# Kernel tuning notes

Measured on AMD Instinct MI355X. Metric: run time of the kernel, lower is better.

Reference implementation:

```python
import jax, jax.numpy as jnp
import numpy as np


def _rbf(X1, X2, log_ls):
    # exp(-||x1-x2||^2 / (2*ls^2)) via the squared-norm expansion
    sq1 = jnp.sum(X1 * X1, axis=-1)[:, None]
    sq2 = jnp.sum(X2 * X2, axis=-1)[None, :]
    d2 = jnp.maximum(sq1 + sq2 - 2.0 * (X1 @ X2.T), 0.0)
    ls2 = jnp.exp(2.0 * log_ls)
    return jnp.exp(-d2 / (2.0 * ls2))


def setup_inputs() -> dict:
    key = jax.random.key(0)
    k1, k2, k3 = jax.random.split(key, 3)
    N_way, K_shot, Q_query, D = 16, 32, 4096, 1024
    Zs = jax.random.normal(k1, (N_way * K_shot, D), dtype=jnp.float32)
    Ys = jax.random.randint(k2, (N_way * K_shot, 1), 0, N_way)
    Zq = jax.random.normal(k3, (N_way * Q_query, D), dtype=jnp.float32)
    log_ls = jnp.asarray(0.0, dtype=jnp.float32)
    log_noise = jnp.asarray(-3.0, dtype=jnp.float32)
    return {"Zs": Zs, "Ys": Ys, "Zq": Zq, "log_ls": log_ls,
            "log_noise": log_noise, "N_way": N_way}


def reference(Zs, Ys, Zq, log_ls, log_noise, N_way):
    Nsamp = Zs.shape[0]  # N_way * K_shot
    Y1hot = jax.nn.one_hot(Ys.reshape(-1), N_way, dtype=Zs.dtype)  # [Nsamp, N_way]
    noise = jnp.exp(2.0 * log_noise)
    Kss = _rbf(Zs, Zs, log_ls) + noise * jnp.eye(Nsamp, dtype=Zs.dtype)
    L = jnp.linalg.cholesky(Kss)
    alpha = jax.scipy.linalg.cho_solve((L, True), Y1hot)  # [Nsamp, N_way]
    Kqs = _rbf(Zq, Zs, log_ls)  # [Q, Nsamp]
    f_q = Kqs @ alpha  # [Q, N_way]
    return jax.nn.softmax(f_q, axis=-1)
```

## Files before the change

### kernel.cpp

```cpp
#include <hip/hip_runtime.h>
#include <math.h>

#define NS 512
#define NQ 65536
#define DD 1024
#define NW 16

typedef __attribute__((ext_vector_type(8))) short short8x;
typedef __attribute__((ext_vector_type(4))) float floatx4;

static __device__ __forceinline__ unsigned short bf_trunc(float x) {
  return (unsigned short)(__float_as_uint(x) >> 16);
}
static __device__ __forceinline__ float bf_tof(unsigned short h) {
  return __uint_as_float(((unsigned)h) << 16);
}
static __device__ __forceinline__ unsigned short bf_rne(float x) {
  unsigned u = __float_as_uint(x);
  return (unsigned short)((u + 0x7FFFu + ((u >> 16) & 1u)) >> 16);
}

#define STASH(Hp, Lp, row, k0, v) do {                                      \
    unsigned e_ = (unsigned)((((row) * 32 + (k0)) ^ (((row) & 7) << 3)));   \
    ushort4 h_, l_;                                                         \
    h_.x = bf_trunc((v).x); l_.x = bf_trunc((v).x - bf_tof(h_.x));          \
    h_.y = bf_trunc((v).y); l_.y = bf_trunc((v).y - bf_tof(h_.y));          \
    h_.z = bf_trunc((v).z); l_.z = bf_trunc((v).z - bf_tof(h_.z));          \
    h_.w = bf_trunc((v).w); l_.w = bf_trunc((v).w - bf_tof(h_.w));          \
    *(ushort4*)&Hp[e_] = h_; *(ushort4*)&Lp[e_] = l_;                       \
  } while (0)

__global__ void row_norms_kernel(const float* __restrict__ X, float* __restrict__ out, int nrows) {
  int gw = (int)((blockIdx.x * blockDim.x + threadIdx.x) >> 6);
  int lane = threadIdx.x & 63;
  if (gw >= nrows) return;
  const float* row = X + (size_t)gw * DD;
  float s = 0.f;
  #pragma unroll
  for (int i = 0; i < 4; ++i) {
    float4 v = *(const float4*)(row + 4 * lane + 256 * i);
    s += v.x * v.x + v.y * v.y + v.z * v.z + v.w * v.w;
  }
  #pragma unroll
  for (int off = 32; off; off >>= 1) s += __shfl_xor(s, off);
  if (lane == 0) out[gw] = s;
}

__global__ __launch_bounds__(256) void kss_kernel(const float* __restrict__ Zs,
                                                  const float* __restrict__ sn,
                                                  const float* __restrict__ log_ls,
                                                  const float* __restrict__ log_noise,
                                                  float* __restrict__ K) {
  __shared__ __align__(16) float At[16][68];
  __shared__ __align__(16) float Bt[16][68];
  int tid = threadIdx.x;
  int rb = blockIdx.y * 64, cb = blockIdx.x * 64;
  int tx = tid & 15, ty = tid >> 4;
  int srow = tid & 63, skq = (tid >> 6) << 2;
  float acc[4][4] = {};
  for (int kk = 0; kk < DD; kk += 16) {
    __syncthreads();
    float4 a = *(const float4*)(Zs + (size_t)(rb + srow) * DD + kk + skq);
    float4 b = *(const float4*)(Zs + (size_t)(cb + srow) * DD + kk + skq);
    At[skq + 0][srow] = a.x; At[skq + 1][srow] = a.y; At[skq + 2][srow] = a.z; At[skq + 3][srow] = a.w;
    Bt[skq + 0][srow] = b.x; Bt[skq + 1][srow] = b.y; Bt[skq + 2][srow] = b.z; Bt[skq + 3][srow] = b.w;
    __syncthreads();
    #pragma unroll
    for (int k = 0; k < 16; ++k) {
      float4 av = *(const float4*)&At[k][ty * 4];
      float4 bv = *(const float4*)&Bt[k][tx * 4];
      float aa[4] = {av.x, av.y, av.z, av.w};
      float bb[4] = {bv.x, bv.y, bv.z, bv.w};
      #pragma unroll
      for (int i = 0; i < 4; ++i)
        #pragma unroll
        for (int j = 0; j < 4; ++j)
          acc[i][j] = fmaf(aa[i], bb[j], acc[i][j]);
    }
  }
  float inv2 = 0.5f * expf(-2.f * log_ls[0]);
  float noise = expf(2.f * log_noise[0]);
  #pragma unroll
  for (int i = 0; i < 4; ++i)
    #pragma unroll
    for (int j = 0; j < 4; ++j) {
      int r = rb + ty * 4 + i, c = cb + tx * 4 + j;
      float d2 = fmaxf(sn[r] + sn[c] - 2.f * acc[i][j], 0.f);
      float v = expf(-d2 * inv2);
      if (r == c) v += noise;
      K[(size_t)r * NS + c] = v;
    }
}

__global__ __launch_bounds__(256) void panel_v2(float* __restrict__ K, int j) {
  __shared__ float Ld[64][68];
  __shared__ float idia_s[64];
  const int tid = threadIdx.x;

  if (tid < 64) {
    const int r = tid;
    float ar[64];
    #pragma unroll
    for (int c4 = 0; c4 < 16; ++c4)
      *(floatx4*)&ar[c4 * 4] = *(const floatx4*)(K + (size_t)(j + r) * NS + j + c4 * 4);
    float myinv = 0.f;
    #pragma unroll
    for (int c = 0; c < 64; ++c) {
      float colv = ar[c];
      float d = __shfl(colv, c);
      float sq = sqrtf(d);
      float inv = 1.f / sq;
      float x = (r > c) ? colv * inv : ((r == c) ? sq : 0.f);
      ar[c] = x;
      if (r == c) myinv = inv;
      #pragma unroll
      for (int k = c + 1; k < 64; ++k) {
        float xk = __shfl(x, k);
        ar[k] = fmaf(-x, xk, ar[k]);
      }
    }
    idia_s[r] = myinv;
    #pragma unroll
    for (int c4 = 0; c4 < 16; ++c4)
      *(floatx4*)&Ld[r][c4 * 4] = *(const floatx4*)&ar[c4 * 4];
    #pragma unroll
    for (int c = 0; c < 64; ++c) {
      if (c <= r) K[(size_t)(j + r) * NS + j + c] = ar[c];
      if (c < r)  K[(size_t)(j + c) * NS + j + r] = ar[c];
    }
  }
  __syncthreads();

  for (int r0 = j + 64 + tid; r0 < NS; r0 += 256) {
    float xr[64];
    #pragma unroll
    for (int c4 = 0; c4 < 16; ++c4)
      *(floatx4*)&xr[c4 * 4] = *(const floatx4*)(K + (size_t)r0 * NS + j + c4 * 4);
    #pragma unroll
    for (int g = 0; g < 16; ++g) {
      float v0 = xr[4 * g + 0], v1 = xr[4 * g + 1], v2 = xr[4 * g + 2], v3 = xr[4 * g + 3];
      for (int kb = 0; kb < g; ++kb) {
        floatx4 x4 = *(const floatx4*)&xr[4 * kb];
        floatx4 l0 = *(const floatx4*)&Ld[4 * g + 0][4 * kb];
        floatx4 l1 = *(const floatx4*)&Ld[4 * g + 1][4 * kb];
        floatx4 l2 = *(const floatx4*)&Ld[4 * g + 2][4 * kb];
        floatx4 l3 = *(const floatx4*)&Ld[4 * g + 3][4 * kb];
        v0 -= x4.x * l0.x + x4.y * l0.y + x4.z * l0.z + x4.w * l0.w;
        v1 -= x4.x * l1.x + x4.y * l1.y + x4.z * l1.z + x4.w * l1.w;
        v2 -= x4.x * l2.x + x4.y * l2.y + x4.z * l2.z + x4.w * l2.w;
        v3 -= x4.x * l3.x + x4.y * l3.y + x4.z * l3.z + x4.w * l3.w;
      }
      const int c0 = 4 * g;
      float x0 = v0 * idia_s[c0 + 0];
      v1 -= x0 * Ld[c0 + 1][c0];
      float x1 = v1 * idia_s[c0 + 1];
      v2 -= x0 * Ld[c0 + 2][c0] + x1 * Ld[c0 + 2][c0 + 1];
      float x2 = v2 * idia_s[c0 + 2];
      v3 -= x0 * Ld[c0 + 3][c0] + x1 * Ld[c0 + 3][c0 + 1] + x2 * Ld[c0 + 3][c0 + 2];
      float x3 = v3 * idia_s[c0 + 3];
      xr[c0 + 0] = x0; xr[c0 + 1] = x1; xr[c0 + 2] = x2; xr[c0 + 3] = x3;
    }
    #pragma unroll
    for (int c4 = 0; c4 < 16; ++c4)
      *(floatx4*)(K + (size_t)r0 * NS + j + c4 * 4) = *(const floatx4*)&xr[c4 * 4];
    #pragma unroll
    for (int c = 0; c < 64; ++c)
      K[(size_t)(j + c) * NS + r0] = xr[c];
  }
}

__global__ __launch_bounds__(256) void syrk_trailing(float* __restrict__ K, int j) {
  int t0 = j + 64;
  int rbt = t0 + blockIdx.y * 64, cbt = t0 + blockIdx.x * 64;
  if (cbt > rbt) return;
  __shared__ float A[64][69];
  __shared__ float B[64][69];
  int tid = threadIdx.x;
  for (int i = tid; i < 64 * 64; i += 256) {
    int r = i >> 6, k = i & 63;
    A[r][k] = K[(size_t)(rbt + r) * NS + j + k];
    B[r][k] = K[(size_t)(cbt + r) * NS + j + k];
  }
  __syncthreads();
  int tx = tid & 15, ty = tid >> 4;
  float acc[4][4] = {};
  for (int k = 0; k < 64; ++k) {
    float aa[4], bb[4];
    #pragma unroll
    for (int i = 0; i < 4; ++i) aa[i] = A[ty * 4 + i][k];
    #pragma unroll
    for (int i = 0; i < 4; ++i) bb[i] = B[tx * 4 + i][k];
    #pragma unroll
    for (int i = 0; i < 4; ++i)
      #pragma unroll
      for (int jj = 0; jj < 4; ++jj)
        acc[i][jj] = fmaf(aa[i], bb[jj], acc[i][jj]);
  }
  #pragma unroll
  for (int i = 0; i < 4; ++i)
    #pragma unroll
    for (int jj = 0; jj < 4; ++jj)
      K[(size_t)(rbt + ty * 4 + i) * NS + cbt + tx * 4 + jj] -= acc[i][jj];
}

__global__ __launch_bounds__(1024) void cho_solve_v2(const float* __restrict__ K,
                                                     const int* __restrict__ Ys,
                                                     unsigned short* __restrict__ alpha_t) {
  __shared__ float P[64][68];
  __shared__ float WsT[16][68];
  __shared__ float Wblk[64][16];
  __shared__ float invd[64];
  const int tid = threadIdx.x;
  const int rs = tid >> 4, nn = tid & 15;
  const int pc = nn * 4;

  float w[8];
  #pragma unroll
  for (int k = 0; k < 8; ++k) w[k] = (Ys[rs + 64 * k] == nn) ? 1.f : 0.f;

  for (int jb = 0; jb < 8; ++jb) {
    const int j = jb << 6;
    __syncthreads();
    #pragma unroll
    for (int k = 0; k < 8; ++k) if (k == jb) Wblk[rs][nn] = w[k];
    *(floatx4*)&P[rs][pc] = *(const floatx4*)(K + (size_t)(j + rs) * NS + j + pc);
    __syncthreads();
    if (tid < 64) {
      const int n = tid & 15, rq = tid >> 4;
      invd[tid] = 1.f / P[tid][tid];
      float w16[16];
      #pragma unroll
      for (int i = 0; i < 16; ++i) w16[i] = Wblk[rq + 4 * i][n];
      #pragma unroll
      for (int g = 0; g < 16; ++g) {
        floatx4 p[16];
        #pragma unroll
        for (int i = 0; i < 16; ++i) p[i] = *(const floatx4*)&P[rq + 4 * i][4 * g];
        #pragma unroll
        for (int cj = 0; cj < 4; ++cj) {
          const int c = 4 * g + cj;
          float xc = __shfl(w16[c >> 2], ((c & 3) << 4) + n) * invd[c];
          if (rq == (c & 3)) w16[c >> 2] = xc;
          #pragma unroll
          for (int i = 0; i < 16; ++i) {
            int r = rq + 4 * i;
            if (r > c) w16[i] -= p[i][cj] * xc;
          }
        }
      }
      #pragma unroll
      for (int i = 0; i < 16; ++i) WsT[n][rq + 4 * i] = w16[i];
    }
    __syncthreads();
    #pragma unroll
    for (int k = 0; k < 8; ++k) if (k == jb) w[k] = WsT[nn][rs];
    floatx4 wsr[16];
    #pragma unroll
    for (int g = 0; g < 16; ++g) wsr[g] = *(const floatx4*)&WsT[nn][4 * g];
    #pragma unroll
    for (int k = 0; k < 8; ++k) {
      if (k > jb) {
        const float* lrow = K + (size_t)(rs + 64 * k) * NS + j;
        float s = w[k];
        #pragma unroll
        for (int g = 0; g < 16; ++g) {
          floatx4 lv = *(const floatx4*)(lrow + 4 * g);
          s -= lv.x * wsr[g].x + lv.y * wsr[g].y + lv.z * wsr[g].z + lv.w * wsr[g].w;
        }
        w[k] = s;
      }
    }
  }

  for (int jb = 7; jb >= 0; --jb) {
    const int j = jb << 6;
    __syncthreads();
    #pragma unroll
    for (int k = 0; k < 8; ++k) if (k == jb) Wblk[rs][nn] = w[k];
    *(floatx4*)&P[rs][pc] = *(const floatx4*)(K + (size_t)(j + rs) * NS + j + pc);
    __syncthreads();
    if (tid < 64) {
      const int n = tid & 15, rq = tid >> 4;
      invd[tid] = 1.f / P[tid][tid];
      float w16[16];
      #pragma unroll
      for (int i = 0; i < 16; ++i) w16[i] = Wblk[rq + 4 * i][n];
      #pragma unroll
      for (int g = 15; g >= 0; --g) {
        floatx4 p[16];
        #pragma unroll
        for (int i = 0; i < 16; ++i) p[i] = *(const floatx4*)&P[rq + 4 * i][4 * g];
        #pragma unroll
        for (int cj = 3; cj >= 0; --cj) {
          const int c = 4 * g + cj;
          float xc = __shfl(w16[c >> 2], ((c & 3) << 4) + n) * invd[c];
          if (rq == (c & 3)) w16[c >> 2] = xc;
          #pragma unroll
          for (int i = 0; i < 16; ++i) {
            int r = rq + 4 * i;
            if (r < c) w16[i] -= p[i][cj] * xc;
          }
        }
      }
      #pragma unroll
      for (int i = 0; i < 16; ++i) WsT[n][rq + 4 * i] = w16[i];
    }
    __syncthreads();
    #pragma unroll
    for (int k = 0; k < 8; ++k) if (k == jb) w[k] = WsT[nn][rs];
    floatx4 wsr[16];
    #pragma unroll
    for (int g = 0; g < 16; ++g) wsr[g] = *(const floatx4*)&WsT[nn][4 * g];
    #pragma unroll
    for (int k = 0; k < 8; ++k) {
      if (k < jb) {
        const float* lrow = K + (size_t)(rs + 64 * k) * NS + j;
        float s = w[k];
        #pragma unroll
        for (int g = 0; g < 16; ++g) {
          floatx4 lv = *(const floatx4*)(lrow + 4 * g);
          s -= lv.x * wsr[g].x + lv.y * wsr[g].y + lv.z * wsr[g].z + lv.w * wsr[g].w;
        }
        w[k] = s;
      }
    }
  }

  #pragma unroll
  for (int k = 0; k < 8; ++k)
    alpha_t[(size_t)nn * NS + rs + 64 * k] = bf_rne(w[k]);
}

__global__ __launch_bounds__(512) void fused_v2(const float* __restrict__ Zq,
                                                const float* __restrict__ Zs,
                                                const float* __restrict__ sn,
                                                const unsigned short* __restrict__ alpha_t,
                                                const float* __restrict__ log_ls,
                                                float* __restrict__ out) {
  __shared__ __align__(16) unsigned short LB[32768];
  __shared__ float qnl[128];
  __shared__ float snl[256];
  unsigned short* AhB = LB;
  unsigned short* AlB = LB + 4096;
  unsigned short* BhB = LB + 8192;
  unsigned short* BlB = LB + 16384;
  unsigned short* KqB = LB;

  const int tid = threadIdx.x;
  const int lane = tid & 63;
  const int w = tid >> 6;
  const int wm = w >> 2, wn = w & 3;
  const int l15 = lane & 15, l4 = lane >> 4;
  const int rb = blockIdx.x * 128;
  const float inv2 = 0.5f * __expf(-2.f * log_ls[0]);
  const unsigned swz = (unsigned)((l15 & 7) << 3);

  if (tid < 128) qnl[tid] = 0.f;
  __syncthreads();

  const int qrow0 = tid >> 3;
  const int qk0 = (tid & 7) * 4;
  const int qrow1 = 64 + qrow0;

  floatx4 facc = {0.f, 0.f, 0.f, 0.f};

  for (int cc = 0; cc < NS; cc += 256) {
    if (tid < 256) snl[tid] = sn[cc + tid];
    floatx4 acc[4][4];
    #pragma unroll
    for (int a = 0; a < 4; ++a)
      #pragma unroll
      for (int b = 0; b < 4; ++b) acc[a][b] = (floatx4){0.f, 0.f, 0.f, 0.f};

    float4 pq0 = *(const float4*)(Zq + (size_t)(rb + qrow0) * DD + qk0);
    float4 pq1 = *(const float4*)(Zq + (size_t)(rb + qrow1) * DD + qk0);
    float4 ps[4];
    #pragma unroll
    for (int u = 0; u < 4; ++u) {
      int idx = tid + (u << 9);
      ps[u] = *(const float4*)(Zs + (size_t)(cc + (idx >> 3)) * DD + ((idx & 7) * 4));
    }

    for (int kt = 0; kt < 32; ++kt) {
      STASH(AhB, AlB, qrow0, qk0, pq0);
      STASH(AhB, AlB, qrow1, qk0, pq1);
      #pragma unroll
      for (int u = 0; u < 4; ++u) {
        int idx = tid + (u << 9);
        int srow = idx >> 3, sk0 = (idx & 7) * 4;
        STASH(BhB, BlB, srow, sk0, ps[u]);
      }
      if (cc == 0) {
        float s0 = pq0.x * pq0.x + pq0.y * pq0.y + pq0.z * pq0.z + pq0.w * pq0.w;
        float s1 = pq1.x * pq1.x + pq1.y * pq1.y + pq1.z * pq1.z + pq1.w * pq1.w;
        #pragma unroll
        for (int d = 1; d < 8; d <<= 1) { s0 += __shfl_xor(s0, d); s1 += __shfl_xor(s1, d); }
        if ((tid & 7) == 0) { qnl[qrow0] += s0; qnl[qrow1] += s1; }
      }
      __syncthreads();
      if (kt < 31) {
        int kk2 = (kt + 1) << 5;
        pq0 = *(const float4*)(Zq + (size_t)(rb + qrow0) * DD + kk2 + qk0);
        pq1 = *(const float4*)(Zq + (size_t)(rb + qrow1) * DD + kk2 + qk0);
        #pragma unroll
        for (int u = 0; u < 4; ++u) {
          int idx = tid + (u << 9);
          ps[u] = *(const float4*)(Zs + (size_t)(cc + (idx >> 3)) * DD + kk2 + ((idx & 7) * 4));
        }
      }
      short8x ah[4], al[4], bh[4], bl[4];
      #pragma unroll
      for (int mi = 0; mi < 4; ++mi) {
        unsigned e = (unsigned)((wm * 64 + mi * 16 + l15) * 32 + 8 * l4) ^ swz;
        ah[mi] = *(const short8x*)&AhB[e];
        al[mi] = *(const short8x*)&AlB[e];
      }
      #pragma unroll
      for (int ni = 0; ni < 4; ++ni) {
        unsigned e = (unsigned)((wn * 64 + ni * 16 + l15) * 32 + 8 * l4) ^ swz;
        bh[ni] = *(const short8x*)&BhB[e];
        bl[ni] = *(const short8x*)&BlB[e];
      }
      #pragma unroll
      for (int mi = 0; mi < 4; ++mi)
        #pragma unroll
        for (int ni = 0; ni < 4; ++ni) {
          acc[mi][ni] = __builtin_amdgcn_mfma_f32_16x16x32_bf16(ah[mi], bh[ni], acc[mi][ni], 0, 0, 0);
          acc[mi][ni] = __builtin_amdgcn_mfma_f32_16x16x32_bf16(ah[mi], bl[ni], acc[mi][ni], 0, 0, 0);
          acc[mi][ni] = __builtin_amdgcn_mfma_f32_16x16x32_bf16(al[mi], bh[ni], acc[mi][ni], 0, 0, 0);
        }
      __syncthreads();
    }

    short8x bfr[8];
    #pragma unroll
    for (int s = 0; s < 8; ++s)
      bfr[s] = *(const short8x*)(alpha_t + ((size_t)l15 * NS + cc + 32 * s + 8 * l4));

    #pragma unroll
    for (int mi = 0; mi < 4; ++mi)
      #pragma unroll
      for (int rr = 0; rr < 4; ++rr) {
        int row_l = wm * 64 + mi * 16 + l4 * 4 + rr;
        float qv = qnl[row_l];
        unsigned sw = (unsigned)((row_l & 7) << 3);
        #pragma unroll
        for (int ni = 0; ni < 4; ++ni) {
          int col = wn * 64 + ni * 16 + l15;
          float d2 = fmaxf(qv + snl[col] - 2.f * acc[mi][ni][rr], 0.f);
          float kq = __expf(-d2 * inv2);
          KqB[(unsigned)(row_l * 256 + col) ^ sw] = bf_rne(kq);
        }
      }
    __syncthreads();
    #pragma unroll
    for (int s = 0; s < 8; ++s) {
      unsigned e = (unsigned)((w * 16 + l15) * 256 + 32 * s + 8 * l4) ^ swz;
      short8x ak = *(const short8x*)&KqB[e];
      facc = __builtin_amdgcn_mfma_f32_16x16x32_bf16(ak, bfr[s], facc, 0, 0, 0);
    }
    __syncthreads();
  }

  #pragma unroll
  for (int r = 0; r < 4; ++r) {
    float v = facc[r];
    float m = v;
    #pragma unroll
    for (int d = 1; d < 16; d <<= 1) m = fmaxf(m, __shfl_xor(m, d));
    float e = __expf(v - m);
    float s = e;
    #pragma unroll
    for (int d = 1; d < 16; d <<= 1) s += __shfl_xor(s, d);
    out[(size_t)(rb + w * 16 + l4 * 4 + r) * NW + l15] = e / s;
  }
}

extern "C" void kernel_launch(void* const* d_in, const int* in_sizes, int n_in,
                              void* d_out, int out_size, void* d_ws, size_t ws_size,
                              hipStream_t stream) {
  (void)in_sizes; (void)n_in; (void)out_size; (void)ws_size;
  const float* Zs = (const float*)d_in[0];
  const int*   Ys = (const int*)d_in[1];
  const float* Zq = (const float*)d_in[2];
  const float* log_ls = (const float*)d_in[3];
  const float* log_noise = (const float*)d_in[4];
  float* out = (float*)d_out;

  float* ws = (float*)d_ws;
  float* K  = ws;
  float* sn = ws + (size_t)NS * NS;
  unsigned short* alpha_t = (unsigned short*)(sn + NS);

  row_norms_kernel<<<128, 256, 0, stream>>>(Zs, sn, NS);
  kss_kernel<<<dim3(8, 8), 256, 0, stream>>>(Zs, sn, log_ls, log_noise, K);
  for (int j = 0; j < NS; j += 64) {
    panel_v2<<<1, 256, 0, stream>>>(K, j);
    int rows = NS - j - 64;
    if (rows > 0) {
      int t = rows / 64;
      syrk_trailing<<<dim3(t, t), 256, 0, stream>>>(K, j);
    }
  }
  cho_solve_v2<<<1, 1024, 0, stream>>>(K, Ys, alpha_t);
  fused_v2<<<NQ / 128, 512, 0, stream>>>(Zq, Zs, sn, alpha_t, log_ls, out);
}
```

Before: 1.478 ms.

## Fuse Cholesky panel, trailing update and next diagonal factorization into one kernel per step

The row-norm, Kss build and first diagonal-tile factorization are merged into one kernel that computes only the lower-triangular tiles. Each later step becomes a single launch: every block redoes the triangular solve for the panel rows it needs, applies the rank-64 trailing update, and block 0 then factors the next diagonal tile. This roughly halves the chain of serialized small launches. Solved panel rows are also written to a contiguous Lrow buffer so the forward solve reads them with unit stride. The cost is redundant triangular-solve work across blocks and extra workspace.

```diff
diff --git a/kernel.cpp b/kernel.cpp
--- a/kernel.cpp
+++ b/kernel.cpp
@@ -30,80 +30,14 @@
     *(ushort4*)&Hp[e_] = h_; *(ushort4*)&Lp[e_] = l_;                       \
   } while (0)
 
-__global__ void row_norms_kernel(const float* __restrict__ X, float* __restrict__ out, int nrows) {
-  int gw = (int)((blockIdx.x * blockDim.x + threadIdx.x) >> 6);
-  int lane = threadIdx.x & 63;
-  if (gw >= nrows) return;
-  const float* row = X + (size_t)gw * DD;
-  float s = 0.f;
-  #pragma unroll
-  for (int i = 0; i < 4; ++i) {
-    float4 v = *(const float4*)(row + 4 * lane + 256 * i);
-    s += v.x * v.x + v.y * v.y + v.z * v.z + v.w * v.w;
-  }
-  #pragma unroll
-  for (int off = 32; off; off >>= 1) s += __shfl_xor(s, off);
-  if (lane == 0) out[gw] = s;
-}
-
-__global__ __launch_bounds__(256) void kss_kernel(const float* __restrict__ Zs,
-                                                  const float* __restrict__ sn,
-                                                  const float* __restrict__ log_ls,
-                                                  const float* __restrict__ log_noise,
-                                                  float* __restrict__ K) {
-  __shared__ __align__(16) float At[16][68];
-  __shared__ __align__(16) float Bt[16][68];
-  int tid = threadIdx.x;
-  int rb = blockIdx.y * 64, cb = blockIdx.x * 64;
-  int tx = tid & 15, ty = tid >> 4;
-  int srow = tid & 63, skq = (tid >> 6) << 2;
-  float acc[4][4] = {};
-  for (int kk = 0; kk < DD; kk += 16) {
-    __syncthreads();
-    float4 a = *(const float4*)(Zs + (size_t)(rb + srow) * DD + kk + skq);
-    float4 b = *(const float4*)(Zs + (size_t)(cb + srow) * DD + kk + skq);
-    At[skq + 0][srow] = a.x; At[skq + 1][srow] = a.y; At[skq + 2][srow] = a.z; At[skq + 3][srow] = a.w;
-    Bt[skq + 0][srow] = b.x; Bt[skq + 1][srow] = b.y; Bt[skq + 2][srow] = b.z; Bt[skq + 3][srow] = b.w;
-    __syncthreads();
-    #pragma unroll
-    for (int k = 0; k < 16; ++k) {
-      float4 av = *(const float4*)&At[k][ty * 4];
-      float4 bv = *(const float4*)&Bt[k][tx * 4];
-      float aa[4] = {av.x, av.y, av.z, av.w};
-      float bb[4] = {bv.x, bv.y, bv.z, bv.w};
-      #pragma unroll
-      for (int i = 0; i < 4; ++i)
-        #pragma unroll
-        for (int j = 0; j < 4; ++j)
-          acc[i][j] = fmaf(aa[i], bb[j], acc[i][j]);
-    }
-  }
-  float inv2 = 0.5f * expf(-2.f * log_ls[0]);
-  float noise = expf(2.f * log_noise[0]);
-  #pragma unroll
-  for (int i = 0; i < 4; ++i)
-    #pragma unroll
-    for (int j = 0; j < 4; ++j) {
-      int r = rb + ty * 4 + i, c = cb + tx * 4 + j;
-      float d2 = fmaxf(sn[r] + sn[c] - 2.f * acc[i][j], 0.f);
-      float v = expf(-d2 * inv2);
-      if (r == c) v += noise;
-      K[(size_t)r * NS + c] = v;
-    }
-}
-
-__global__ __launch_bounds__(256) void panel_v2(float* __restrict__ K, int j) {
-  __shared__ float Ld[64][68];
-  __shared__ float idia_s[64];
+__device__ __forceinline__ void potrf_tile(const float* T68, float* __restrict__ K, int j) {
   const int tid = threadIdx.x;
-
   if (tid < 64) {
     const int r = tid;
     float ar[64];
     #pragma unroll
     for (int c4 = 0; c4 < 16; ++c4)
-      *(floatx4*)&ar[c4 * 4] = *(const floatx4*)(K + (size_t)(j + r) * NS + j + c4 * 4);
-    float myinv = 0.f;
+      *(floatx4*)&ar[c4 * 4] = *(const floatx4*)&T68[r * 68 + c4 * 4];
     #pragma unroll
     for (int c = 0; c < 64; ++c) {
       float colv = ar[c];
@@ -112,98 +46,210 @@
       float inv = 1.f / sq;
       float x = (r > c) ? colv * inv : ((r == c) ? sq : 0.f);
       ar[c] = x;
-      if (r == c) myinv = inv;
       #pragma unroll
       for (int k = c + 1; k < 64; ++k) {
         float xk = __shfl(x, k);
         ar[k] = fmaf(-x, xk, ar[k]);
       }
     }
-    idia_s[r] = myinv;
-    #pragma unroll
-    for (int c4 = 0; c4 < 16; ++c4)
-      *(floatx4*)&Ld[r][c4 * 4] = *(const floatx4*)&ar[c4 * 4];
     #pragma unroll
     for (int c = 0; c < 64; ++c) {
       if (c <= r) K[(size_t)(j + r) * NS + j + c] = ar[c];
       if (c < r)  K[(size_t)(j + c) * NS + j + r] = ar[c];
     }
   }
+}
+
+__device__ __forceinline__ void trsm_row(const float* __restrict__ Krow,
+                                         const float* Ld, const float* invd,
+                                         float* xr) {
+  #pragma unroll
+  for (int c4 = 0; c4 < 16; ++c4)
+    *(floatx4*)&xr[c4 * 4] = *(const floatx4*)(Krow + c4 * 4);
+  #pragma unroll
+  for (int g = 0; g < 16; ++g) {
+    float v0 = xr[4 * g + 0], v1 = xr[4 * g + 1], v2 = xr[4 * g + 2], v3 = xr[4 * g + 3];
+    for (int kb = 0; kb < g; ++kb) {
+      floatx4 x4 = *(const floatx4*)&xr[4 * kb];
+      floatx4 l0 = *(const floatx4*)&Ld[(4 * g + 0) * 68 + 4 * kb];
+      floatx4 l1 = *(const floatx4*)&Ld[(4 * g + 1) * 68 + 4 * kb];
+      floatx4 l2 = *(const floatx4*)&Ld[(4 * g + 2) * 68 + 4 * kb];
+      floatx4 l3 = *(const floatx4*)&Ld[(4 * g + 3) * 68 + 4 * kb];
+      v0 -= x4.x * l0.x + x4.y * l0.y + x4.z * l0.z + x4.w * l0.w;
+      v1 -= x4.x * l1.x + x4.y * l1.y + x4.z * l1.z + x4.w * l1.w;
+      v2 -= x4.x * l2.x + x4.y * l2.y + x4.z * l2.z + x4.w * l2.w;
+      v3 -= x4.x * l3.x + x4.y * l3.y + x4.z * l3.z + x4.w * l3.w;
+    }
+    const int c0 = 4 * g;
+    float x0 = v0 * invd[c0];
+    v1 -= x0 * Ld[(c0 + 1) * 68 + c0];
+    float x1 = v1 * invd[c0 + 1];
+    v2 -= x0 * Ld[(c0 + 2) * 68 + c0] + x1 * Ld[(c0 + 2) * 68 + c0 + 1];
+    float x2 = v2 * invd[c0 + 2];
+    v3 -= x0 * Ld[(c0 + 3) * 68 + c0] + x1 * Ld[(c0 + 3) * 68 + c0 + 1] + x2 * Ld[(c0 + 3) * 68 + c0 + 2];
+    float x3 = v3 * invd[c0 + 3];
+    xr[c0] = x0; xr[c0 + 1] = x1; xr[c0 + 2] = x2; xr[c0 + 3] = x3;
+  }
+}
+
+__global__ __launch_bounds__(256) void kss_p0(const float* __restrict__ Zs,
+                                              const float* __restrict__ log_ls,
+                                              const float* __restrict__ log_noise,
+                                              float* __restrict__ K,
+                                              float* __restrict__ sn) {
+  __shared__ float snl[128];
+  __shared__ __align__(16) float At[16][68];
+  __shared__ __align__(16) float Bt[16][68];
+  __shared__ __align__(16) float Tile[64][68];
+  const int wg = blockIdx.x, tid = threadIdx.x;
+  int by = 0, accv = 0;
+  while (accv + by + 1 <= wg) { accv += by + 1; ++by; }
+  const int bx = wg - accv;
+  const int rb = by * 64, cb = bx * 64;
+
+  if (tid < 128) {
+    int row = (tid < 64) ? rb + tid : cb + (tid - 64);
+    const float4* rp = (const float4*)(Zs + (size_t)row * DD);
+    float s0 = 0.f, s1 = 0.f, s2 = 0.f, s3 = 0.f;
+    for (int i = 0; i < 256; i += 4) {
+      float4 a = rp[i], b2 = rp[i + 1], c2 = rp[i + 2], d2 = rp[i + 3];
+      s0 += a.x * a.x + a.y * a.y + a.z * a.z + a.w * a.w;
+      s1 += b2.x * b2.x + b2.y * b2.y + b2.z * b2.z + b2.w * b2.w;
+      s2 += c2.x * c2.x + c2.y * c2.y + c2.z * c2.z + c2.w * c2.w;
+      s3 += d2.x * d2.x + d2.y * d2.y + d2.z * d2.z + d2.w * d2.w;
+    }
+    snl[tid] = (s0 + s1) + (s2 + s3);
+    if (by == bx && tid < 64) sn[rb + tid] = snl[tid];
+  }
+  const int tx = tid & 15, ty = tid >> 4;
+  const int srow = tid & 63, skq = (tid >> 6) << 2;
+  float acc[4][4] = {};
+  for (int kk = 0; kk < DD; kk += 16) {
+    __syncthreads();
+    float4 a = *(const float4*)(Zs + (size_t)(rb + srow) * DD + kk + skq);
+    float4 b = *(const float4*)(Zs + (size_t)(cb + srow) * DD + kk + skq);
+    At[skq + 0][srow] = a.x; At[skq + 1][srow] = a.y;
+    At[skq + 2][srow] = a.z; At[skq + 3][srow] = a.w;
+    Bt[skq + 0][srow] = b.x; Bt[skq + 1][srow] = b.y;
+    Bt[skq + 2][srow] = b.z; Bt[skq + 3][srow] = b.w;
+    __syncthreads();
+    #pragma unroll
+    for (int k = 0; k < 16; ++k) {
+      floatx4 av = *(const floatx4*)&At[k][ty * 4];
+      floatx4 bv = *(const floatx4*)&Bt[k][tx * 4];
+      #pragma unroll
+      for (int i = 0; i < 4; ++i)
+        #pragma unroll
+        for (int jj = 0; jj < 4; ++jj)
+          acc[i][jj] = fmaf(av[i], bv[jj], acc[i][jj]);
+    }
+  }
+  float inv2 = 0.5f * expf(-2.f * log_ls[0]);
+  float noise = expf(2.f * log_noise[0]);
+  #pragma unroll
+  for (int i = 0; i < 4; ++i)
+    #pragma unroll
+    for (int jj = 0; jj < 4; ++jj) {
+      int rl = ty * 4 + i, cl = tx * 4 + jj;
+      int r = rb + rl, c = cb + cl;
+      float d2 = fmaxf(snl[rl] + snl[64 + cl] - 2.f * acc[i][jj], 0.f);
+      float v = expf(-d2 * inv2);
+      if (r == c) v += noise;
+      K[(size_t)r * NS + c] = v;
+      if (wg == 0) Tile[rl][cl] = v;
+    }
+  if (wg == 0) {
+    __syncthreads();
+    potrf_tile(&Tile[0][0], K, 0);
+  }
+}
+
+__global__ __launch_bounds__(256) void panel_step(float* __restrict__ K,
+                                                  float* __restrict__ Lrow,
+                                                  int jb) {
+  __shared__ float Ld[64 * 68];
+  __shared__ float A_[64 * 68];
+  __shared__ float B_[64 * 68];
+  __shared__ float invd[64];
+  const int tid = threadIdx.x;
+  const int j = jb << 6;
+  int ti = 0, a2 = 0;
+  while (a2 + ti + 1 <= (int)blockIdx.x) { a2 += ti + 1; ++ti; }
+  const int tj = (int)blockIdx.x - a2;
+  const int rbt = j + 64 + ti * 64, cbt = j + 64 + tj * 64;
+  float* A = A_;
+  float* B = (ti == tj) ? A_ : B_;
+
+  #pragma unroll
+  for (int it = 0; it < 4; ++it) {
+    int flat = tid + 256 * it;
+    int r = flat >> 4, c4 = (flat & 15) * 4;
+    *(floatx4*)&Ld[r * 68 + c4] = *(const floatx4*)&K[(size_t)(j + r) * NS + j + c4];
+  }
   __syncthreads();
-
-  for (int r0 = j + 64 + tid; r0 < NS; r0 += 256) {
+  if (tid < 64) invd[tid] = 1.f / Ld[tid * 68 + tid];
+  __syncthreads();
+
+  if (tid < 64) {
     float xr[64];
+    const int row = rbt + tid;
+    trsm_row(&K[(size_t)row * NS + j], Ld, invd, xr);
     #pragma unroll
     for (int c4 = 0; c4 < 16; ++c4)
-      *(floatx4*)&xr[c4 * 4] = *(const floatx4*)(K + (size_t)r0 * NS + j + c4 * 4);
-    #pragma unroll
-    for (int g = 0; g < 16; ++g) {
-      float v0 = xr[4 * g + 0], v1 = xr[4 * g + 1], v2 = xr[4 * g + 2], v3 = xr[4 * g + 3];
-      for (int kb = 0; kb < g; ++kb) {
-        floatx4 x4 = *(const floatx4*)&xr[4 * kb];
-        floatx4 l0 = *(const floatx4*)&Ld[4 * g + 0][4 * kb];
-        floatx4 l1 = *(const floatx4*)&Ld[4 * g + 1][4 * kb];
-        floatx4 l2 = *(const floatx4*)&Ld[4 * g + 2][4 * kb];
-        floatx4 l3 = *(const floatx4*)&Ld[4 * g + 3][4 * kb];
-        v0 -= x4.x * l0.x + x4.y * l0.y + x4.z * l0.z + x4.w * l0.w;
-        v1 -= x4.x * l1.x + x4.y * l1.y + x4.z * l1.z + x4.w * l1.w;
-        v2 -= x4.x * l2.x + x4.y * l2.y + x4.z * l2.z + x4.w * l2.w;
-        v3 -= x4.x * l3.x + x4.y * l3.y + x4.z * l3.z + x4.w * l3.w;
-      }
-      const int c0 = 4 * g;
-      float x0 = v0 * idia_s[c0 + 0];
-      v1 -= x0 * Ld[c0 + 1][c0];
-      float x1 = v1 * idia_s[c0 + 1];
-      v2 -= x0 * Ld[c0 + 2][c0] + x1 * Ld[c0 + 2][c0 + 1];
-      float x2 = v2 * idia_s[c0 + 2];
-      v3 -= x0 * Ld[c0 + 3][c0] + x1 * Ld[c0 + 3][c0 + 1] + x2 * Ld[c0 + 3][c0 + 2];
-      float x3 = v3 * idia_s[c0 + 3];
-      xr[c0 + 0] = x0; xr[c0 + 1] = x1; xr[c0 + 2] = x2; xr[c0 + 3] = x3;
-    }
+      *(floatx4*)&A[tid * 68 + c4 * 4] = *(const floatx4*)&xr[c4 * 4];
+    if (tj == 0) {
+      float* lr = Lrow + ((size_t)jb * NS + row) * 64;
+      #pragma unroll
+      for (int c4 = 0; c4 < 16; ++c4)
+        *(floatx4*)(lr + c4 * 4) = *(const floatx4*)&xr[c4 * 4];
+      #pragma unroll
+      for (int c = 0; c < 64; ++c)
+        K[(size_t)(j + c) * NS + row] = xr[c];
+    }
+  } else if (tid < 128 && ti != tj) {
+    float xr[64];
+    const int row = cbt + (tid - 64);
+    trsm_row(&K[(size_t)row * NS + j], Ld, invd, xr);
     #pragma unroll
     for (int c4 = 0; c4 < 16; ++c4)
-      *(floatx4*)(K + (size_t)r0 * NS + j + c4 * 4) = *(const floatx4*)&xr[c4 * 4];
-    #pragma unroll
-    for (int c = 0; c < 64; ++c)
-      K[(size_t)(j + c) * NS + r0] = xr[c];
-  }
-}
-
-__global__ __launch_bounds__(256) void syrk_trailing(float* __restrict__ K, int j) {
-  int t0 = j + 64;
-  int rbt = t0 + blockIdx.y * 64, cbt = t0 + blockIdx.x * 64;
-  if (cbt > rbt) return;
-  __shared__ float A[64][69];
-  __shared__ float B[64][69];
-  int tid = threadIdx.x;
-  for (int i = tid; i < 64 * 64; i += 256) {
-    int r = i >> 6, k = i & 63;
-    A[r][k] = K[(size_t)(rbt + r) * NS + j + k];
-    B[r][k] = K[(size_t)(cbt + r) * NS + j + k];
+      *(floatx4*)&B[(tid - 64) * 68 + c4 * 4] = *(const floatx4*)&xr[c4 * 4];
   }
   __syncthreads();
-  int tx = tid & 15, ty = tid >> 4;
-  float acc[4][4] = {};
-  for (int k = 0; k < 64; ++k) {
-    float aa[4], bb[4];
-    #pragma unroll
-    for (int i = 0; i < 4; ++i) aa[i] = A[ty * 4 + i][k];
-    #pragma unroll
-    for (int i = 0; i < 4; ++i) bb[i] = B[tx * 4 + i][k];
+
+  {
+    const int tx = tid & 15, ty = tid >> 4;
+    float acc[4][4] = {};
+    for (int k = 0; k < 64; ++k) {
+      float aa[4], bb[4];
+      #pragma unroll
+      for (int i = 0; i < 4; ++i) aa[i] = A[(ty * 4 + i) * 68 + k];
+      #pragma unroll
+      for (int i = 0; i < 4; ++i) bb[i] = B[(tx * 4 + i) * 68 + k];
+      #pragma unroll
+      for (int i = 0; i < 4; ++i)
+        #pragma unroll
+        for (int jj = 0; jj < 4; ++jj)
+          acc[i][jj] = fmaf(aa[i], bb[jj], acc[i][jj]);
+    }
+    __syncthreads();
     #pragma unroll
     for (int i = 0; i < 4; ++i)
       #pragma unroll
-      for (int jj = 0; jj < 4; ++jj)
-        acc[i][jj] = fmaf(aa[i], bb[jj], acc[i][jj]);
-  }
-  #pragma unroll
-  for (int i = 0; i < 4; ++i)
-    #pragma unroll
-    for (int jj = 0; jj < 4; ++jj)
-      K[(size_t)(rbt + ty * 4 + i) * NS + cbt + tx * 4 + jj] -= acc[i][jj];
-}
-
-__global__ __launch_bounds__(1024) void cho_solve_v2(const float* __restrict__ K,
+      for (int jj = 0; jj < 4; ++jj) {
+        float* cp = &K[(size_t)(rbt + ty * 4 + i) * NS + cbt + tx * 4 + jj];
+        float nv = *cp - acc[i][jj];
+        *cp = nv;
+        if (blockIdx.x == 0) Ld[(ty * 4 + i) * 68 + tx * 4 + jj] = nv;
+      }
+  }
+  if (blockIdx.x == 0) {
+    __syncthreads();
+    potrf_tile(Ld, K, j + 64);
+  }
+}
+
+__global__ __launch_bounds__(1024) void cho_solve_v4(const float* __restrict__ K,
+                                                     const float* __restrict__ Lrow,
                                                      const int* __restrict__ Ys,
                                                      unsigned short* __restrict__ alpha_t) {
   __shared__ float P[64][68];
@@ -260,7 +306,7 @@
     #pragma unroll
     for (int k = 0; k < 8; ++k) {
       if (k > jb) {
-        const float* lrow = K + (size_t)(rs + 64 * k) * NS + j;
+        const float* lrow = Lrow + ((size_t)jb * NS + rs + 64 * k) * 64;
         float s = w[k];
         #pragma unroll
         for (int g = 0; g < 16; ++g) {
@@ -489,19 +535,16 @@
 
   float* ws = (float*)d_ws;
   float* K  = ws;
-  float* sn = ws + (size_t)NS * NS;
+  float* sn = K + (size_t)NS * NS;
   unsigned short* alpha_t = (unsigned short*)(sn + NS);
-
-  row_norms_kernel<<<128, 256, 0, stream>>>(Zs, sn, NS);
-  kss_kernel<<<dim3(8, 8), 256, 0, stream>>>(Zs, sn, log_ls, log_noise, K);
-  for (int j = 0; j < NS; j += 64) {
-    panel_v2<<<1, 256, 0, stream>>>(K, j);
-    int rows = NS - j - 64;
-    if (rows > 0) {
-      int t = rows / 64;
-      syrk_trailing<<<dim3(t, t), 256, 0, stream>>>(K, j);
-    }
-  }
-  cho_solve_v2<<<1, 1024, 0, stream>>>(K, Ys, alpha_t);
+  float* Lrow = sn + NS + 4096;
+
+  kss_p0<<<36, 256, 0, stream>>>(Zs, log_ls, log_noise, K, sn);
+  for (int jb = 0; jb < 7; ++jb) {
+    int T = 7 - jb;
+    int nt = T * (T + 1) / 2;
+    panel_step<<<nt, 256, 0, stream>>>(K, Lrow, jb);
+  }
+  cho_solve_v4<<<1, 1024, 0, stream>>>(K, Lrow, Ys, alpha_t);
   fused_v2<<<NQ / 128, 512, 0, stream>>>(Zq, Zs, sn, alpha_t, log_ls, out);
 }
```

After: 1.707 ms. 1.16x slower.
